# Optimization experiments

Hardware: AMD Instinct MI355X
Metric: run time of the kernel (lower is better)

## Reference

```python
import jax, jax.numpy as jnp
import numpy as np

B, L, D, H, R = 2, 128, 256, 8, 4
DK = D // H  # 32
EPS = 1e-6


def setup_inputs() -> dict:
    key = jax.random.key(0)
    ks = jax.random.split(key, 12)
    q = jax.random.normal(ks[0], (B, L, D), jnp.float32)
    k = jax.random.normal(ks[1], (B, L, D), jnp.float32)
    v = jax.random.normal(ks[2], (B, L, D), jnp.float32)
    t = jnp.sort(jax.random.uniform(ks[3], (B, L), jnp.float32), axis=-1)
    omega = jax.random.uniform(ks[4], (B, L, L), jnp.float32)
    mask = jnp.triu(jnp.ones((L, L), bool), 1)  # True = masked (causal)
    xav = (2.0 / (D + D)) ** 0.5
    Wq = jax.random.normal(ks[5], (D, H * DK), jnp.float32) * xav
    Wk = jax.random.normal(ks[6], (D, H * DK), jnp.float32) * xav
    Wv = jax.random.normal(ks[7], (D, H * DK), jnp.float32) * xav
    s = jax.random.uniform(ks[8], (R,), jnp.float32) + 0.1  # ODE time-decay scales
    fc_w = jax.random.normal(ks[9], (H * DK, D), jnp.float32) * xav
    fc_b = jnp.zeros((D,), jnp.float32)
    ln_g = jnp.ones((D,), jnp.float32)
    ln_b = jnp.zeros((D,), jnp.float32)
    return {"q": q, "k": k, "v": v, "t": t, "omega": omega, "mask": mask,
            "Wq": Wq, "Wk": Wk, "Wv": Wv, "s": s,
            "fc_w": fc_w, "fc_b": fc_b, "ln_g": ln_g, "ln_b": ln_b}


def _ode_proj(x, W, phi):
    # x: (B,L,D), W: (D,H*DK), phi: (B,L,L,R) time kernel
    p = x @ W                                       # (B,L,H*DK)
    y = p[:, None, :, None, :] * phi[..., None]     # (B,L,L,R,H*DK)
    y = y.reshape(B, L, L, R, H, DK)
    return y.transpose(0, 4, 1, 2, 3, 5)            # (B,H,L,L,R,DK)


def reference(q, k, v, t, omega, mask, Wq, Wk, Wv, s, fc_w, fc_b, ln_g, ln_b):
    temp = DK ** 0.5
    residual = q
    # pre-LayerNorm on q (normalize_before=True)
    mu = q.mean(-1, keepdims=True)
    var = q.var(-1, keepdims=True)
    qn = (q - mu) / jnp.sqrt(var + EPS) * ln_g + ln_b
    # continuous-time kernel phi[b,i,j,r] = exp(-|t_i - t_j| * s_r)
    dt = jnp.abs(t[:, :, None] - t[:, None, :])     # (B,L,L)
    phi = jnp.exp(-dt[..., None] * s)               # (B,L,L,R)
    q6 = _ode_proj(qn, Wq, phi)                     # (B,H,L,L,R,DK)
    k6 = _ode_proj(k, Wk, phi)
    v6 = _ode_proj(v, Wv, phi)
    # attn = (q/temp * k * omega).sum(-1).sum(-1)
    attn = jnp.einsum('bhijrd,bhijrd,bij->bhij', q6 / temp, k6, omega)
    attn = jnp.where(mask[None, None, :, :], -1e9, attn)
    attn = jax.nn.softmax(attn, axis=-1)            # (B,H,L,L)
    vsum = v6.sum(axis=4)                           # sum over R -> (B,H,L,L,DK)
    out = jnp.einsum('bhij,bhijd->bhid', attn, vsum)  # (B,H,L,DK)
    out = out.transpose(0, 2, 1, 3).reshape(B, L, H * DK)
    out = out @ fc_w + fc_b + residual              # dropout = identity (eval)
    return (out, attn)
```

## Files before the change

### kernel.cpp

```cpp
#include <hip/hip_runtime.h>

#define B_  2
#define L_  128
#define D_  256
#define H_  8
#define R_  4
#define DK_ 32
#define BL_ (B_*L_)

__device__ __forceinline__ float wredsum64(float v) {
    #pragma unroll
    for (int m = 32; m >= 1; m >>= 1) v += __shfl_xor(v, m, 64);
    return v;
}
__device__ __forceinline__ float wredmax64(float v) {
    #pragma unroll
    for (int m = 32; m >= 1; m >>= 1) v = fmaxf(v, __shfl_xor(v, m, 64));
    return v;
}

__global__ __launch_bounds__(256) void k_proj(
    const float* __restrict__ q, const float* __restrict__ k, const float* __restrict__ v,
    const float* __restrict__ Wq, const float* __restrict__ Wk, const float* __restrict__ Wv,
    const float* __restrict__ ln_g, const float* __restrict__ ln_b,
    float* __restrict__ pv, float* __restrict__ qkdot)
{
    const int blk = blockIdx.x;
    const int row = blk >> 2;
    const int cg  = blk & 3;
    const int tid = threadIdx.x;

    __shared__ __align__(16) float sx[3][D_];
    __shared__ __align__(16) float part[16][3][64];
    __shared__ float red[8];
    __shared__ float spq[64], spk[64];

    if (tid < 192) {
        const int which = tid >> 6, f4 = tid & 63;
        const float* src = (which == 0) ? q : (which == 1) ? k : v;
        reinterpret_cast<float4*>(sx[which])[f4] =
            reinterpret_cast<const float4*>(src + (size_t)row * D_)[f4];
    }
    __syncthreads();

    {
        const float qv = sx[0][tid];
        float s1 = qv, s2 = qv * qv;
        #pragma unroll
        for (int m = 32; m >= 1; m >>= 1) {
            s1 += __shfl_xor(s1, m, 64);
            s2 += __shfl_xor(s2, m, 64);
        }
        if ((tid & 63) == 0) { red[(tid >> 6) * 2] = s1; red[(tid >> 6) * 2 + 1] = s2; }
    }
    __syncthreads();
    {
        const float mu  = (red[0] + red[2] + red[4] + red[6]) * (1.0f / D_);
        const float msq = (red[1] + red[3] + red[5] + red[7]) * (1.0f / D_);
        const float var = msq - mu * mu;
        const float qn = (sx[0][tid] - mu) * rsqrtf(var + 1e-6f) * ln_g[tid] + ln_b[tid];
        __syncthreads();
        sx[0][tid] = qn;
    }
    __syncthreads();

    const int c4  = tid & 15;
    const int kg  = tid >> 4;
    const int gc4 = cg * 16 + c4;
    const int kbase = kg * 16;
    {
        const float4* W4 = reinterpret_cast<const float4*>(Wq);
        float4 a = {0,0,0,0};
        #pragma unroll
        for (int kk = 0; kk < 16; ++kk) {
            const int r = kbase + kk;
            const float x = sx[0][r];
            const float4 w = W4[r * 64 + gc4];
            a.x += x * w.x; a.y += x * w.y; a.z += x * w.z; a.w += x * w.w;
        }
        reinterpret_cast<float4*>(part[kg][0])[c4] = a;
    }
    {
        const float4* W4 = reinterpret_cast<const float4*>(Wk);
        float4 a = {0,0,0,0};
        #pragma unroll
        for (int kk = 0; kk < 16; ++kk) {
            const int r = kbase + kk;
            const float x = sx[1][r];
            const float4 w = W4[r * 64 + gc4];
            a.x += x * w.x; a.y += x * w.y; a.z += x * w.z; a.w += x * w.w;
        }
        reinterpret_cast<float4*>(part[kg][1])[c4] = a;
    }
    {
        const float4* W4 = reinterpret_cast<const float4*>(Wv);
        float4 a = {0,0,0,0};
        #pragma unroll
        for (int kk = 0; kk < 16; ++kk) {
            const int r = kbase + kk;
            const float x = sx[2][r];
            const float4 w = W4[r * 64 + gc4];
            a.x += x * w.x; a.y += x * w.y; a.z += x * w.z; a.w += x * w.w;
        }
        reinterpret_cast<float4*>(part[kg][2])[c4] = a;
    }
    __syncthreads();

    if (tid < 192) {
        const int m = tid >> 6, c = tid & 63;
        float sum = 0.f;
        #pragma unroll
        for (int g = 0; g < 16; ++g) sum += part[g][m][c];
        if      (m == 0) spq[c] = sum;
        else if (m == 1) spk[c] = sum;
        else             pv[(size_t)row * D_ + cg * 64 + c] = sum;
    }
    __syncthreads();

    if (tid < 64) {
        float d = spq[tid] * spk[tid];
        #pragma unroll
        for (int m = 16; m >= 1; m >>= 1) d += __shfl_xor(d, m, 64);
        if ((tid & 31) == 0)
            qkdot[(size_t)row * H_ + cg * 2 + (tid >> 5)] = d;
    }
}

__global__ __launch_bounds__(256) void k_attn(
    const float* __restrict__ t, const float* __restrict__ omega, const float* __restrict__ s,
    const float* __restrict__ pv, const float* __restrict__ qkdot,
    float* __restrict__ mid, float* __restrict__ dout)
{
    const int blk = blockIdx.x;
    const int b  = blk >> 9;
    const int i  = (blk >> 2) & (L_ - 1);
    const int cg = blk & 3;
    const int tid = threadIdx.x;

    __shared__ __align__(16) float sQK[L_ * H_];
    __shared__ __align__(16) float sOm[L_];
    __shared__ __align__(16) float sAttn[2][L_];
    __shared__ __align__(16) float part[16][64];
    __shared__ float sPhi[L_], sPsi[L_], sS[R_];

    if (tid < R_) sS[tid] = s[tid];
    reinterpret_cast<float4*>(sQK)[tid] =
        reinterpret_cast<const float4*>(qkdot + (size_t)b * L_ * H_)[tid];
    if (tid < 32)
        reinterpret_cast<float4*>(sOm)[tid] =
            reinterpret_cast<const float4*>(omega + ((size_t)(b * L_ + i)) * L_)[tid];
    __syncthreads();

    if (tid < L_) {
        const float dtv = fabsf(t[b * L_ + i] - t[b * L_ + tid]);
        float Phi = 0.f, Psi = 0.f;
        #pragma unroll
        for (int r = 0; r < R_; ++r) {
            const float e = expf(-dtv * sS[r]);
            Phi += e;
            Psi += e * e;
        }
        sPhi[tid] = Phi;
        sPsi[tid] = Psi;
    }
    __syncthreads();

    const int w = tid >> 6, lane = tid & 63;
    const float invtemp = 0.17677669529663687f;
    if (w < 2) {
        const int h = cg * 2 + w;
        const int j0 = lane, j1 = lane + 64;
        float l0 = (j0 <= i) ? sOm[j0] * sPsi[j0] * sQK[j0 * H_ + h] * invtemp : -3.0e38f;
        float l1 = (j1 <= i) ? sOm[j1] * sPsi[j1] * sQK[j1 * H_ + h] * invtemp : -3.0e38f;
        const float mx = wredmax64(fmaxf(l0, l1));
        const float e0 = (j0 <= i) ? expf(l0 - mx) : 0.f;
        const float e1 = (j1 <= i) ? expf(l1 - mx) : 0.f;
        const float inv = 1.0f / wredsum64(e0 + e1);
        const float a0 = e0 * inv, a1 = e1 * inv;
        sAttn[w][j0] = a0;
        sAttn[w][j1] = a1;
        const size_t ab = (size_t)BL_ * D_ + (((size_t)(b * H_ + h) * L_ + i) * L_);
        dout[ab + j0] = a0;
        dout[ab + j1] = a1;
    }
    __syncthreads();

    const int c4  = tid & 15;
    const int jg  = tid >> 4;
    const int gc4 = cg * 16 + c4;
    const int hl  = (gc4 >> 3) & 1;
    const float4* pv4 = reinterpret_cast<const float4*>(pv + (size_t)b * L_ * D_);
    float4 acc = {0,0,0,0};
    for (int j = jg; j <= i; j += 16) {
        const float wgt = sAttn[hl][j] * sPhi[j];
        const float4 p = pv4[j * 64 + gc4];
        acc.x += wgt * p.x; acc.y += wgt * p.y; acc.z += wgt * p.z; acc.w += wgt * p.w;
    }
    reinterpret_cast<float4*>(part[jg])[c4] = acc;
    __syncthreads();
    if (tid < 64) {
        float sum = 0.f;
        #pragma unroll
        for (int g = 0; g < 16; ++g) sum += part[g][tid];
        mid[((size_t)(b * L_ + i)) * D_ + cg * 64 + tid] = sum;
    }
}

__global__ __launch_bounds__(256) void k_fc(
    const float* __restrict__ q, const float* __restrict__ fc_w, const float* __restrict__ fc_b,
    const float* __restrict__ mid, float* __restrict__ dout)
{
    const int blk = blockIdx.x;
    const int row = blk >> 2;
    const int cg  = blk & 3;
    const int tid = threadIdx.x;

    __shared__ __align__(16) float sMid[D_];
    __shared__ __align__(16) float part[16][64];

    if (tid < 64)
        reinterpret_cast<float4*>(sMid)[tid] =
            reinterpret_cast<const float4*>(mid + (size_t)row * D_)[tid];
    __syncthreads();

    const int c4  = tid & 15;
    const int kg  = tid >> 4;
    const int gc4 = cg * 16 + c4;
    const int kbase = kg * 16;
    const float4* fw4 = reinterpret_cast<const float4*>(fc_w);
    float4 a = {0,0,0,0};
    #pragma unroll
    for (int kk = 0; kk < 16; ++kk) {
        const int r = kbase + kk;
        const float x = sMid[r];
        const float4 w = fw4[r * 64 + gc4];
        a.x += x * w.x; a.y += x * w.y; a.z += x * w.z; a.w += x * w.w;
    }
    reinterpret_cast<float4*>(part[kg])[c4] = a;
    __syncthreads();

    if (tid < 64) {
        const int c = cg * 64 + tid;
        float sum = fc_b[c] + q[(size_t)row * D_ + c];
        #pragma unroll
        for (int g = 0; g < 16; ++g) sum += part[g][tid];
        dout[(size_t)row * D_ + c] = sum;
    }
}

extern "C" void kernel_launch(void* const* d_in, const int* in_sizes, int n_in,
                              void* d_out, int out_size, void* d_ws, size_t ws_size,
                              hipStream_t stream) {
    const float* q     = (const float*)d_in[0];
    const float* k     = (const float*)d_in[1];
    const float* v     = (const float*)d_in[2];
    const float* t     = (const float*)d_in[3];
    const float* omega = (const float*)d_in[4];
    const float* Wq    = (const float*)d_in[6];
    const float* Wk    = (const float*)d_in[7];
    const float* Wv    = (const float*)d_in[8];
    const float* s     = (const float*)d_in[9];
    const float* fc_w  = (const float*)d_in[10];
    const float* fc_b  = (const float*)d_in[11];
    const float* ln_g  = (const float*)d_in[12];
    const float* ln_b  = (const float*)d_in[13];

    float* ws    = (float*)d_ws;
    float* pv    = ws;
    float* qkdot = ws + 65536;
    float* mid   = ws + 67584;
    float* out   = (float*)d_out;

    hipLaunchKernelGGL(k_proj, dim3(4 * BL_), dim3(256), 0, stream,
                       q, k, v, Wq, Wk, Wv, ln_g, ln_b, pv, qkdot);
    hipLaunchKernelGGL(k_attn, dim3(4 * BL_), dim3(256), 0, stream,
                       t, omega, s, pv, qkdot, mid, out);
    hipLaunchKernelGGL(k_fc, dim3(4 * BL_), dim3(256), 0, stream,
                       q, fc_w, fc_b, mid, out);
}
```

Baseline: 99.97 us.

## Tile projection, attention and FC kernels over 4 rows for weight reuse

The projection and FC kernels now process 4 rows per block over 16-column slices, so each weight load is reused across 4 rows instead of one. The attention kernel handles one head for 4 query rows per block, reusing each pv load across those rows and summing the per-head qk partial dot products from a finer 16-way split. Cross-row reuse should cut global and L2 traffic for weights and pv. In exchange there are more block barriers in the projection loop, larger shared memory, and the attention reduction now runs over all 128 j for every row instead of stopping at the causal limit.

New measurement: 95.71 us. 1.04x faster.

```diff
diff --git a/kernel.cpp b/kernel.cpp
--- a/kernel.cpp
+++ b/kernel.cpp
@@ -7,6 +7,7 @@
 #define R_  4
 #define DK_ 32
 #define BL_ (B_*L_)
+#define SXP 260
 
 __device__ __forceinline__ float wredsum64(float v) {
     #pragma unroll
@@ -23,136 +24,131 @@
     const float* __restrict__ q, const float* __restrict__ k, const float* __restrict__ v,
     const float* __restrict__ Wq, const float* __restrict__ Wk, const float* __restrict__ Wv,
     const float* __restrict__ ln_g, const float* __restrict__ ln_b,
-    float* __restrict__ pv, float* __restrict__ qkdot)
+    float* __restrict__ pv, float* __restrict__ qkpart)
 {
     const int blk = blockIdx.x;
-    const int row = blk >> 2;
-    const int cg  = blk & 3;
+    const int rowTile = blk >> 4;
+    const int cg = blk & 15;
+    const int rbase = rowTile * 4;
     const int tid = threadIdx.x;
 
-    __shared__ __align__(16) float sx[3][D_];
-    __shared__ __align__(16) float part[16][3][64];
-    __shared__ float red[8];
-    __shared__ float spq[64], spk[64];
-
-    if (tid < 192) {
-        const int which = tid >> 6, f4 = tid & 63;
-        const float* src = (which == 0) ? q : (which == 1) ? k : v;
-        reinterpret_cast<float4*>(sx[which])[f4] =
-            reinterpret_cast<const float4*>(src + (size_t)row * D_)[f4];
-    }
-    __syncthreads();
-
-    {
-        const float qv = sx[0][tid];
-        float s1 = qv, s2 = qv * qv;
+    __shared__ __align__(16) float sx[3][4 * SXP];
+    __shared__ __align__(16) float partF[16 * 4 * 16];
+    __shared__ float spq[4][16], spk[4][16];
+
+    {
+        const int r = tid >> 6, f4c = tid & 63;
+        #pragma unroll
+        for (int p = 0; p < 3; ++p) {
+            const float* src = (p == 0 ? q : (p == 1 ? k : v)) + (size_t)(rbase + r) * D_;
+            *reinterpret_cast<float4*>(&sx[p][r * SXP + f4c * 4]) =
+                reinterpret_cast<const float4*>(src)[f4c];
+        }
+    }
+    __syncthreads();
+
+    {
+        const int r = tid >> 6, lane = tid & 63;
+        float x0 = sx[0][r * SXP + lane];
+        float x1 = sx[0][r * SXP + lane + 64];
+        float x2 = sx[0][r * SXP + lane + 128];
+        float x3 = sx[0][r * SXP + lane + 192];
+        float s1 = x0 + x1 + x2 + x3;
+        float s2 = x0*x0 + x1*x1 + x2*x2 + x3*x3;
         #pragma unroll
         for (int m = 32; m >= 1; m >>= 1) {
             s1 += __shfl_xor(s1, m, 64);
             s2 += __shfl_xor(s2, m, 64);
         }
-        if ((tid & 63) == 0) { red[(tid >> 6) * 2] = s1; red[(tid >> 6) * 2 + 1] = s2; }
-    }
-    __syncthreads();
-    {
-        const float mu  = (red[0] + red[2] + red[4] + red[6]) * (1.0f / D_);
-        const float msq = (red[1] + red[3] + red[5] + red[7]) * (1.0f / D_);
-        const float var = msq - mu * mu;
-        const float qn = (sx[0][tid] - mu) * rsqrtf(var + 1e-6f) * ln_g[tid] + ln_b[tid];
+        const float mu = s1 * (1.0f / D_);
+        const float rs = rsqrtf(s2 * (1.0f / D_) - mu * mu + 1e-6f);
+        sx[0][r * SXP + lane      ] = (x0 - mu) * rs * ln_g[lane      ] + ln_b[lane      ];
+        sx[0][r * SXP + lane +  64] = (x1 - mu) * rs * ln_g[lane +  64] + ln_b[lane +  64];
+        sx[0][r * SXP + lane + 128] = (x2 - mu) * rs * ln_g[lane + 128] + ln_b[lane + 128];
+        sx[0][r * SXP + lane + 192] = (x3 - mu) * rs * ln_g[lane + 192] + ln_b[lane + 192];
+    }
+    __syncthreads();
+
+    const int kg  = tid >> 4;
+    const int row = (tid >> 2) & 3;
+    const int c4  = tid & 3;
+    const int gc4 = cg * 4 + c4;
+    const int kbase = kg * 16;
+
+    #pragma unroll
+    for (int m = 0; m < 3; ++m) {
+        const float4* W4 = reinterpret_cast<const float4*>(m == 0 ? Wq : (m == 1 ? Wk : Wv));
+        float4 a = {0, 0, 0, 0};
+        #pragma unroll
+        for (int kk = 0; kk < 16; ++kk) {
+            const int kr = kbase + kk;
+            const float x = sx[m][row * SXP + kr];
+            const float4 w = W4[kr * 64 + gc4];
+            a.x += x * w.x; a.y += x * w.y; a.z += x * w.z; a.w += x * w.w;
+        }
+        *reinterpret_cast<float4*>(&partF[(kg * 16 + row * 4 + c4) * 4]) = a;
         __syncthreads();
-        sx[0][tid] = qn;
-    }
-    __syncthreads();
-
-    const int c4  = tid & 15;
-    const int kg  = tid >> 4;
-    const int gc4 = cg * 16 + c4;
-    const int kbase = kg * 16;
-    {
-        const float4* W4 = reinterpret_cast<const float4*>(Wq);
-        float4 a = {0,0,0,0};
-        #pragma unroll
-        for (int kk = 0; kk < 16; ++kk) {
-            const int r = kbase + kk;
-            const float x = sx[0][r];
-            const float4 w = W4[r * 64 + gc4];
-            a.x += x * w.x; a.y += x * w.y; a.z += x * w.z; a.w += x * w.w;
-        }
-        reinterpret_cast<float4*>(part[kg][0])[c4] = a;
-    }
-    {
-        const float4* W4 = reinterpret_cast<const float4*>(Wk);
-        float4 a = {0,0,0,0};
-        #pragma unroll
-        for (int kk = 0; kk < 16; ++kk) {
-            const int r = kbase + kk;
-            const float x = sx[1][r];
-            const float4 w = W4[r * 64 + gc4];
-            a.x += x * w.x; a.y += x * w.y; a.z += x * w.z; a.w += x * w.w;
-        }
-        reinterpret_cast<float4*>(part[kg][1])[c4] = a;
-    }
-    {
-        const float4* W4 = reinterpret_cast<const float4*>(Wv);
-        float4 a = {0,0,0,0};
-        #pragma unroll
-        for (int kk = 0; kk < 16; ++kk) {
-            const int r = kbase + kk;
-            const float x = sx[2][r];
-            const float4 w = W4[r * 64 + gc4];
-            a.x += x * w.x; a.y += x * w.y; a.z += x * w.z; a.w += x * w.w;
-        }
-        reinterpret_cast<float4*>(part[kg][2])[c4] = a;
-    }
-    __syncthreads();
-
-    if (tid < 192) {
-        const int m = tid >> 6, c = tid & 63;
-        float sum = 0.f;
-        #pragma unroll
-        for (int g = 0; g < 16; ++g) sum += part[g][m][c];
-        if      (m == 0) spq[c] = sum;
-        else if (m == 1) spk[c] = sum;
-        else             pv[(size_t)row * D_ + cg * 64 + c] = sum;
-    }
-    __syncthreads();
+        if (tid < 64) {
+            const int rr = tid >> 4, cc = tid & 15;
+            float sum = 0.f;
+            #pragma unroll
+            for (int g = 0; g < 16; ++g) sum += partF[g * 64 + rr * 16 + cc];
+            if      (m == 0) spq[rr][cc] = sum;
+            else if (m == 1) spk[rr][cc] = sum;
+            else             pv[(size_t)(rbase + rr) * D_ + cg * 16 + cc] = sum;
+        }
+        __syncthreads();
+    }
 
     if (tid < 64) {
-        float d = spq[tid] * spk[tid];
-        #pragma unroll
-        for (int m = 16; m >= 1; m >>= 1) d += __shfl_xor(d, m, 64);
-        if ((tid & 31) == 0)
-            qkdot[(size_t)row * H_ + cg * 2 + (tid >> 5)] = d;
+        const int rr = tid >> 4, cc = tid & 15;
+        float d = spq[rr][cc] * spk[rr][cc];
+        #pragma unroll
+        for (int m = 8; m >= 1; m >>= 1) d += __shfl_xor(d, m, 64);
+        if (cc == 0) qkpart[(size_t)(rbase + rr) * 16 + cg] = d;
     }
 }
 
 __global__ __launch_bounds__(256) void k_attn(
     const float* __restrict__ t, const float* __restrict__ omega, const float* __restrict__ s,
-    const float* __restrict__ pv, const float* __restrict__ qkdot,
+    const float* __restrict__ pv, const float* __restrict__ qkpart,
     float* __restrict__ mid, float* __restrict__ dout)
 {
     const int blk = blockIdx.x;
-    const int b  = blk >> 9;
-    const int i  = (blk >> 2) & (L_ - 1);
-    const int cg = blk & 3;
+    const int b     = blk >> 8;
+    const int itile = (blk >> 3) & 31;
+    const int h     = blk & 7;
+    const int ibase = itile * 4;
     const int tid = threadIdx.x;
 
-    __shared__ __align__(16) float sQK[L_ * H_];
-    __shared__ __align__(16) float sOm[L_];
-    __shared__ __align__(16) float sAttn[2][L_];
-    __shared__ __align__(16) float part[16][64];
-    __shared__ float sPhi[L_], sPsi[L_], sS[R_];
-
-    if (tid < R_) sS[tid] = s[tid];
-    reinterpret_cast<float4*>(sQK)[tid] =
-        reinterpret_cast<const float4*>(qkdot + (size_t)b * L_ * H_)[tid];
-    if (tid < 32)
-        reinterpret_cast<float4*>(sOm)[tid] =
-            reinterpret_cast<const float4*>(omega + ((size_t)(b * L_ + i)) * L_)[tid];
-    __syncthreads();
-
-    if (tid < L_) {
-        const float dtv = fabsf(t[b * L_ + i] - t[b * L_ + tid]);
+    __shared__ __align__(16) float sQKp[L_ * 16];
+    __shared__ __align__(16) float sQKh[L_];
+    __shared__ __align__(16) float sOm[4 * L_];
+    __shared__ __align__(16) float sPhi[4 * L_], sPsi[4 * L_];
+    __shared__ __align__(16) float sAttn[4 * L_];
+    __shared__ __align__(16) float partF[32 * 4 * 32];
+    __shared__ float st[L_], sS[R_];
+
+    {
+        const float4* qkp4 = reinterpret_cast<const float4*>(qkpart + (size_t)b * L_ * 16);
+        reinterpret_cast<float4*>(sQKp)[tid]       = qkp4[tid];
+        reinterpret_cast<float4*>(sQKp)[tid + 256] = qkp4[tid + 256];
+        if (tid < 128)
+            reinterpret_cast<float4*>(sOm)[tid] =
+                reinterpret_cast<const float4*>(omega + ((size_t)(b * L_ + ibase)) * L_)[tid];
+        if (tid < 32)
+            reinterpret_cast<float4*>(st)[tid] =
+                reinterpret_cast<const float4*>(t + (size_t)b * L_)[tid];
+        if (tid < R_) sS[tid] = s[tid];
+    }
+    __syncthreads();
+
+    if (tid < 128) sQKh[tid] = sQKp[tid * 16 + 2 * h] + sQKp[tid * 16 + 2 * h + 1];
+    #pragma unroll
+    for (int p = 0; p < 2; ++p) {
+        const int idx = tid + p * 256;
+        const int w = idx >> 7, j = idx & 127;
+        const float dtv = fabsf(st[ibase + w] - st[j]);
         float Phi = 0.f, Psi = 0.f;
         #pragma unroll
         for (int r = 0; r < R_; ++r) {
@@ -160,49 +156,60 @@
             Phi += e;
             Psi += e * e;
         }
-        sPhi[tid] = Phi;
-        sPsi[tid] = Psi;
+        sPhi[idx] = Phi;
+        sPsi[idx] = Psi;
     }
     __syncthreads();
 
     const int w = tid >> 6, lane = tid & 63;
-    const float invtemp = 0.17677669529663687f;
-    if (w < 2) {
-        const int h = cg * 2 + w;
+    const int i = ibase + w;
+    {
+        const float invtemp = 0.17677669529663687f;
         const int j0 = lane, j1 = lane + 64;
-        float l0 = (j0 <= i) ? sOm[j0] * sPsi[j0] * sQK[j0 * H_ + h] * invtemp : -3.0e38f;
-        float l1 = (j1 <= i) ? sOm[j1] * sPsi[j1] * sQK[j1 * H_ + h] * invtemp : -3.0e38f;
+        float l0 = (j0 <= i) ? sOm[w*L_ + j0] * sPsi[w*L_ + j0] * sQKh[j0] * invtemp : -3.0e38f;
+        float l1 = (j1 <= i) ? sOm[w*L_ + j1] * sPsi[w*L_ + j1] * sQKh[j1] * invtemp : -3.0e38f;
         const float mx = wredmax64(fmaxf(l0, l1));
         const float e0 = (j0 <= i) ? expf(l0 - mx) : 0.f;
         const float e1 = (j1 <= i) ? expf(l1 - mx) : 0.f;
         const float inv = 1.0f / wredsum64(e0 + e1);
         const float a0 = e0 * inv, a1 = e1 * inv;
-        sAttn[w][j0] = a0;
-        sAttn[w][j1] = a1;
+        sAttn[w*L_ + j0] = a0;
+        sAttn[w*L_ + j1] = a1;
         const size_t ab = (size_t)BL_ * D_ + (((size_t)(b * H_ + h) * L_ + i) * L_);
         dout[ab + j0] = a0;
         dout[ab + j1] = a1;
     }
     __syncthreads();
 
-    const int c4  = tid & 15;
-    const int jg  = tid >> 4;
-    const int gc4 = cg * 16 + c4;
-    const int hl  = (gc4 >> 3) & 1;
-    const float4* pv4 = reinterpret_cast<const float4*>(pv + (size_t)b * L_ * D_);
-    float4 acc = {0,0,0,0};
-    for (int j = jg; j <= i; j += 16) {
-        const float wgt = sAttn[hl][j] * sPhi[j];
-        const float4 p = pv4[j * 64 + gc4];
-        acc.x += wgt * p.x; acc.y += wgt * p.y; acc.z += wgt * p.z; acc.w += wgt * p.w;
-    }
-    reinterpret_cast<float4*>(part[jg])[c4] = acc;
-    __syncthreads();
-    if (tid < 64) {
+    {
+        const int jg = tid >> 3, c4 = tid & 7;
+        const int gc4 = h * 8 + c4;
+        const float4* pv4 = reinterpret_cast<const float4*>(pv + (size_t)b * L_ * D_);
+        float4 acc[4];
+        #pragma unroll
+        for (int ww = 0; ww < 4; ++ww) acc[ww] = make_float4(0, 0, 0, 0);
+        #pragma unroll
+        for (int jj = 0; jj < 4; ++jj) {
+            const int j = jg + jj * 32;
+            const float4 p = pv4[j * 64 + gc4];
+            #pragma unroll
+            for (int ww = 0; ww < 4; ++ww) {
+                const float wgt = sAttn[ww*L_ + j] * sPhi[ww*L_ + j];
+                acc[ww].x += wgt * p.x; acc[ww].y += wgt * p.y;
+                acc[ww].z += wgt * p.z; acc[ww].w += wgt * p.w;
+            }
+        }
+        #pragma unroll
+        for (int ww = 0; ww < 4; ++ww)
+            *reinterpret_cast<float4*>(&partF[(jg * 32 + ww * 8 + c4) * 4]) = acc[ww];
+    }
+    __syncthreads();
+    if (tid < 128) {
+        const int ww = tid >> 5, cc = tid & 31;
         float sum = 0.f;
         #pragma unroll
-        for (int g = 0; g < 16; ++g) sum += part[g][tid];
-        mid[((size_t)(b * L_ + i)) * D_ + cg * 64 + tid] = sum;
+        for (int g = 0; g < 32; ++g) sum += partF[g * 128 + ww * 32 + cc];
+        mid[((size_t)(b * L_ + ibase + ww)) * D_ + h * 32 + cc] = sum;
     }
 }
 
@@ -211,40 +218,45 @@
     const float* __restrict__ mid, float* __restrict__ dout)
 {
     const int blk = blockIdx.x;
-    const int row = blk >> 2;
-    const int cg  = blk & 3;
+    const int rowTile = blk >> 4;
+    const int cg = blk & 15;
+    const int rbase = rowTile * 4;
     const int tid = threadIdx.x;
 
-    __shared__ __align__(16) float sMid[D_];
-    __shared__ __align__(16) float part[16][64];
-
-    if (tid < 64)
-        reinterpret_cast<float4*>(sMid)[tid] =
-            reinterpret_cast<const float4*>(mid + (size_t)row * D_)[tid];
-    __syncthreads();
-
-    const int c4  = tid & 15;
+    __shared__ __align__(16) float smid[4 * SXP];
+    __shared__ __align__(16) float partF[16 * 4 * 16];
+
+    {
+        const int r = tid >> 6, f4c = tid & 63;
+        *reinterpret_cast<float4*>(&smid[r * SXP + f4c * 4]) =
+            reinterpret_cast<const float4*>(mid + (size_t)(rbase + r) * D_)[f4c];
+    }
+    __syncthreads();
+
     const int kg  = tid >> 4;
-    const int gc4 = cg * 16 + c4;
+    const int row = (tid >> 2) & 3;
+    const int c4  = tid & 3;
+    const int gc4 = cg * 4 + c4;
     const int kbase = kg * 16;
     const float4* fw4 = reinterpret_cast<const float4*>(fc_w);
-    float4 a = {0,0,0,0};
+    float4 a = {0, 0, 0, 0};
     #pragma unroll
     for (int kk = 0; kk < 16; ++kk) {
-        const int r = kbase + kk;
-        const float x = sMid[r];
-        const float4 w = fw4[r * 64 + gc4];
-        a.x += x * w.x; a.y += x * w.y; a.z += x * w.z; a.w += x * w.w;
-    }
-    reinterpret_cast<float4*>(part[kg])[c4] = a;
+        const int kr = kbase + kk;
+        const float x = smid[row * SXP + kr];
+        const float4 wv = fw4[kr * 64 + gc4];
+        a.x += x * wv.x; a.y += x * wv.y; a.z += x * wv.z; a.w += x * wv.w;
+    }
+    *reinterpret_cast<float4*>(&partF[(kg * 16 + row * 4 + c4) * 4]) = a;
     __syncthreads();
 
     if (tid < 64) {
-        const int c = cg * 64 + tid;
-        float sum = fc_b[c] + q[(size_t)row * D_ + c];
-        #pragma unroll
-        for (int g = 0; g < 16; ++g) sum += part[g][tid];
-        dout[(size_t)row * D_ + c] = sum;
+        const int rr = tid >> 4, cc = tid & 15;
+        const int col = cg * 16 + cc;
+        float sum = fc_b[col] + q[(size_t)(rbase + rr) * D_ + col];
+        #pragma unroll
+        for (int g = 0; g < 16; ++g) sum += partF[g * 64 + rr * 16 + cc];
+        dout[(size_t)(rbase + rr) * D_ + col] = sum;
     }
 }
 
@@ -265,16 +277,16 @@
     const float* ln_g  = (const float*)d_in[12];
     const float* ln_b  = (const float*)d_in[13];
 
-    float* ws    = (float*)d_ws;
-    float* pv    = ws;
-    float* qkdot = ws + 65536;
-    float* mid   = ws + 67584;
-    float* out   = (float*)d_out;
-
-    hipLaunchKernelGGL(k_proj, dim3(4 * BL_), dim3(256), 0, stream,
-                       q, k, v, Wq, Wk, Wv, ln_g, ln_b, pv, qkdot);
-    hipLaunchKernelGGL(k_attn, dim3(4 * BL_), dim3(256), 0, stream,
-                       t, omega, s, pv, qkdot, mid, out);
-    hipLaunchKernelGGL(k_fc, dim3(4 * BL_), dim3(256), 0, stream,
+    float* ws     = (float*)d_ws;
+    float* pv     = ws;
+    float* qkpart = ws + 65536;
+    float* mid    = ws + 69632;
+    float* out    = (float*)d_out;
+
+    hipLaunchKernelGGL(k_proj, dim3(1024), dim3(256), 0, stream,
+                       q, k, v, Wq, Wk, Wv, ln_g, ln_b, pv, qkpart);
+    hipLaunchKernelGGL(k_attn, dim3(512), dim3(256), 0, stream,
+                       t, omega, s, pv, qkpart, mid, out);
+    hipLaunchKernelGGL(k_fc, dim3(1024), dim3(256), 0, stream,
                        q, fc_w, fc_b, mid, out);
 }
```
